# Optimization experiments

Measured on AMD Instinct MI355X. Metric: run time of the kernel, lower is better.

Reference implementation:

```python
import jax, jax.numpy as jnp
import numpy as np

N_NODES = 100000


def _graph_conv(x, W, b, src, dst, n_nodes):
    # DGL GraphConv, norm='both':
    #   h = x * out_deg(src)^{-1/2}; h = h @ W; agg = scatter_sum over dst;
    #   out = agg * in_deg(dst)^{-1/2} + b
    ones = jnp.ones(src.shape, dtype=x.dtype)
    out_deg = jax.ops.segment_sum(ones, src, num_segments=n_nodes)
    in_deg = jax.ops.segment_sum(ones, dst, num_segments=n_nodes)
    norm_src = jax.lax.rsqrt(jnp.maximum(out_deg, 1.0))  # [N]
    norm_dst = jax.lax.rsqrt(jnp.maximum(in_deg, 1.0))   # [N]
    h = (x * norm_src[:, None]) @ W                      # [N, hid]
    msgs = h[src]                                        # [E, hid] gather
    agg = jax.ops.segment_sum(msgs, dst, num_segments=n_nodes)  # [N, hid]
    return jax.nn.relu(agg * norm_dst[:, None] + b)


def setup_inputs() -> dict:
    key = jax.random.key(0)
    k1, k2, k3, k4, k5 = jax.random.split(key, 5)
    n, e, d = N_NODES, 1600000, 128
    x = jax.random.normal(k1, (n, d), dtype=jnp.float32)
    src = jax.random.randint(k2, (e,), 0, n, dtype=jnp.int32)
    dst = jax.random.randint(k3, (e,), 0, n, dtype=jnp.int32)
    # Xavier-ish init for GraphConv weights, zero bias (DGL default)
    W1 = jax.random.normal(k4, (d, d), dtype=jnp.float32) / np.sqrt(d)
    W2 = jax.random.normal(k5, (d, d), dtype=jnp.float32) / np.sqrt(d)
    b1 = jnp.zeros((d,), dtype=jnp.float32)
    b2 = jnp.zeros((d,), dtype=jnp.float32)
    return {"x": x, "W1": W1, "b1": b1, "W2": W2, "b2": b2, "src": src, "dst": dst}


def reference(x, W1, b1, W2, b2, src, dst):
    h = _graph_conv(x, W1, b1, src, dst, N_NODES)
    h = _graph_conv(h, W2, b2, src, dst, N_NODES)
    return h
```

## Files before the change

### kernel.cpp

```cpp
#include <hip/hip_runtime.h>
#include <hip/hip_fp16.h>

#define HD 128
#define CHUNK 4096
#define MAXNB 512

__global__ __launch_bounds__(256) void count_src4(const int* __restrict__ src,
                                                  unsigned int* __restrict__ cnt4s,
                                                  int N, int E) {
    int t = blockIdx.x * 256 + threadIdx.x;
    int e0 = t * 4;
    if (e0 >= E) return;
    if (e0 + 3 < E) {
        int4 s4 = ((const int4*)src)[t];
        atomicAdd(&cnt4s[0 * N + s4.x], 1u);
        atomicAdd(&cnt4s[1 * N + s4.y], 1u);
        atomicAdd(&cnt4s[2 * N + s4.z], 1u);
        atomicAdd(&cnt4s[3 * N + s4.w], 1u);
    } else {
        for (int j = 0; e0 + j < E; ++j)
            atomicAdd(&cnt4s[j * N + src[e0 + j]], 1u);
    }
}

__global__ __launch_bounds__(256) void make_norm_src(const unsigned int* __restrict__ cnt4s,
                                                     float* __restrict__ norm_src, int N) {
    int i = blockIdx.x * 256 + threadIdx.x;
    if (i < N) {
        float od = (float)(cnt4s[i] + cnt4s[N + i] + cnt4s[2 * N + i] + cnt4s[3 * N + i]);
        norm_src[i] = rsqrtf(od > 1.f ? od : 1.f);
    }
}

__global__ __launch_bounds__(256) void hist_coarse(const int* __restrict__ dst,
                                                   unsigned int* __restrict__ gHist,
                                                   int NB, int NC, int E) {
    __shared__ unsigned int hist[MAXNB];
    for (int b = threadIdx.x; b < NB; b += 256) hist[b] = 0;
    __syncthreads();
    int chunk = blockIdx.x;
    int base = chunk * CHUNK;
    int end = base + CHUNK < E ? base + CHUNK : E;
    for (int e = base + threadIdx.x; e < end; e += 256)
        atomicAdd(&hist[dst[e] >> 8], 1u);
    __syncthreads();
    for (int b = threadIdx.x; b < NB; b += 256)
        gHist[(size_t)b * NC + chunk] = hist[b];
}

__global__ __launch_bounds__(256) void scan_a(const unsigned int* __restrict__ cnt,
                                              unsigned int* __restrict__ excl,
                                              unsigned int* __restrict__ bsum, int n) {
    int i = blockIdx.x * 256 + threadIdx.x;
    unsigned int v = (i < n) ? cnt[i] : 0u;
    unsigned int x = v;
#pragma unroll
    for (int d = 1; d < 64; d <<= 1) {
        unsigned int y = __shfl_up(x, d, 64);
        if ((threadIdx.x & 63) >= d) x += y;
    }
    __shared__ unsigned int wsum[4];
    if ((threadIdx.x & 63) == 63) wsum[threadIdx.x >> 6] = x;
    __syncthreads();
    unsigned int woff = 0;
    for (int w = 0; w < (int)(threadIdx.x >> 6); ++w) woff += wsum[w];
    unsigned int incl = x + woff;
    if (i < n) excl[i] = incl - v;
    if (threadIdx.x == 255) bsum[blockIdx.x] = incl;
}

__global__ __launch_bounds__(1024) void scan_b(const unsigned int* __restrict__ bsum,
                                               unsigned int* __restrict__ boff, int nb) {
    int t = threadIdx.x;
    unsigned int v = (t < nb) ? bsum[t] : 0u;
    unsigned int x = v;
#pragma unroll
    for (int d = 1; d < 64; d <<= 1) {
        unsigned int y = __shfl_up(x, d, 64);
        if ((t & 63) >= d) x += y;
    }
    __shared__ unsigned int wsum[16];
    if ((t & 63) == 63) wsum[t >> 6] = x;
    __syncthreads();
    unsigned int woff = 0;
    for (int w = 0; w < (t >> 6); ++w) woff += wsum[w];
    unsigned int incl = x + woff;
    if (t < nb) boff[t] = incl - v;
}

__global__ __launch_bounds__(256) void scan_c(unsigned int* __restrict__ excl,
                                              const unsigned int* __restrict__ boff, int n) {
    int i = blockIdx.x * 256 + threadIdx.x;
    if (i < n) excl[i] += boff[blockIdx.x];
}

__global__ __launch_bounds__(256) void scatter_coarse(const int* __restrict__ src,
                                                      const int* __restrict__ dst,
                                                      const unsigned int* __restrict__ scanA,
                                                      unsigned int* __restrict__ packed,
                                                      int NB, int NC, int E) {
    __shared__ unsigned int curs[MAXNB];
    int chunk = blockIdx.x;
    for (int b = threadIdx.x; b < NB; b += 256)
        curs[b] = scanA[(size_t)b * NC + chunk];
    __syncthreads();
    int base = chunk * CHUNK;
    int end = base + CHUNK < E ? base + CHUNK : E;
    for (int e = base + threadIdx.x; e < end; e += 256) {
        int d = dst[e];
        int s = src[e];
        unsigned int pos = atomicAdd(&curs[d >> 8], 1u);
        packed[pos] = ((unsigned int)(d & 255) << 24) | (unsigned int)s;
    }
}

__global__ __launch_bounds__(256) void fine_sort(const unsigned int* __restrict__ packed,
                                                 const unsigned int* __restrict__ scanA,
                                                 int* __restrict__ sorted_src,
                                                 unsigned int* __restrict__ offsets,
                                                 unsigned int* __restrict__ cntg,
                                                 float* __restrict__ normd,
                                                 int NB, int NC, int N, int E) {
    __shared__ unsigned int cnt[256];
    __shared__ unsigned int curs[256];
    __shared__ unsigned int wsum[4];
    int b = blockIdx.x;
    int t = threadIdx.x;
    unsigned int S = scanA[(size_t)b * NC];
    unsigned int T = (b + 1 < NB) ? scanA[(size_t)(b + 1) * NC] : (unsigned int)E;
    cnt[t] = 0;
    __syncthreads();
    for (unsigned int j = S + t; j < T; j += 256)
        atomicAdd(&cnt[packed[j] >> 24], 1u);
    __syncthreads();
    unsigned int v = cnt[t], x = v;
    int lane = t & 63;
#pragma unroll
    for (int d = 1; d < 64; d <<= 1) {
        unsigned int y = __shfl_up(x, d, 64);
        if (lane >= d) x += y;
    }
    if (lane == 63) wsum[t >> 6] = x;
    __syncthreads();
    unsigned int woff = 0;
    for (int w = 0; w < (t >> 6); ++w) woff += wsum[w];
    unsigned int ex = x - v + woff;
    curs[t] = ex;
    int node = b * 256 + t;
    if (node < N) {
        offsets[node] = S + ex;
        cntg[node] = v;
        float f = (float)v;
        normd[node] = rsqrtf(f > 1.f ? f : 1.f);
    }
    __syncthreads();
    for (unsigned int j = S + t; j < T; j += 256) {
        unsigned int p = packed[j];
        unsigned int pos = S + atomicAdd(&curs[p >> 24], 1u);
        sorted_src[pos] = (int)(p & 0xFFFFFFu);
    }
}

__global__ __launch_bounds__(256) void gemm_norm(const float* __restrict__ x,
                                                 const float* __restrict__ norm,
                                                 const float* __restrict__ W,
                                                 __half* __restrict__ h, int n) {
    __shared__ float Ws[HD * HD];
    __shared__ float xs[32][HD];
    const float4* W4 = (const float4*)W;
    float4* Ws4 = (float4*)Ws;
#pragma unroll
    for (int i = 0; i < 16; ++i)
        Ws4[threadIdx.x + 256 * i] = W4[threadIdx.x + 256 * i];

    const int tid  = threadIdx.x;
    const int row0 = blockIdx.x * 32;

    {
        int r  = tid >> 3;
        int c0 = (tid & 7) * 4;
        int row = row0 + r;
        float nrm = (row < n) ? norm[row] : 0.f;
        const float4* xr = (const float4*)(x + (size_t)row * HD);
        float4* xd = (float4*)xs[r];
#pragma unroll
        for (int j = 0; j < 4; ++j) {
            float4 v = (row < n) ? xr[c0 + j] : make_float4(0.f, 0.f, 0.f, 0.f);
            v.x *= nrm; v.y *= nrm; v.z *= nrm; v.w *= nrm;
            xd[c0 + j] = v;
        }
    }
    __syncthreads();

    const int g  = tid >> 5;
    const int c4 = tid & 31;

    float4 a0 = make_float4(0.f,0.f,0.f,0.f), a1 = a0, a2 = a0, a3 = a0;
#pragma unroll 4
    for (int k = 0; k < HD; ++k) {
        float4 wv = Ws4[k * 32 + c4];
        float x0 = xs[g * 4 + 0][k];
        float x1 = xs[g * 4 + 1][k];
        float x2 = xs[g * 4 + 2][k];
        float x3 = xs[g * 4 + 3][k];
        a0.x = fmaf(x0, wv.x, a0.x); a0.y = fmaf(x0, wv.y, a0.y);
        a0.z = fmaf(x0, wv.z, a0.z); a0.w = fmaf(x0, wv.w, a0.w);
        a1.x = fmaf(x1, wv.x, a1.x); a1.y = fmaf(x1, wv.y, a1.y);
        a1.z = fmaf(x1, wv.z, a1.z); a1.w = fmaf(x1, wv.w, a1.w);
        a2.x = fmaf(x2, wv.x, a2.x); a2.y = fmaf(x2, wv.y, a2.y);
        a2.z = fmaf(x2, wv.z, a2.z); a2.w = fmaf(x2, wv.w, a2.w);
        a3.x = fmaf(x3, wv.x, a3.x); a3.y = fmaf(x3, wv.y, a3.y);
        a3.z = fmaf(x3, wv.z, a3.z); a3.w = fmaf(x3, wv.w, a3.w);
    }

#pragma unroll
    for (int j = 0; j < 4; ++j) {
        int row = row0 + g * 4 + j;
        if (row >= n) break;
        float4 a = (j == 0) ? a0 : (j == 1) ? a1 : (j == 2) ? a2 : a3;
        __half2 lo = __floats2half2_rn(a.x, a.y);
        __half2 hi = __floats2half2_rn(a.z, a.w);
        uint2 pk;
        pk.x = *(unsigned int*)&lo;
        pk.y = *(unsigned int*)&hi;
        ((uint2*)(h + (size_t)row * HD))[c4] = pk;
    }
}

__global__ __launch_bounds__(256) void aggregate(const __half* __restrict__ h,
                                                 const int* __restrict__ sorted_src,
                                                 const unsigned int* __restrict__ offsets,
                                                 const unsigned int* __restrict__ cnt,
                                                 const float* __restrict__ norm_dst,
                                                 const float* __restrict__ bias,
                                                 float* __restrict__ out, int n) {
    int node = blockIdx.x * 4 + (int)(threadIdx.x >> 6);
    if (node >= n) return;
    int lane = threadIdx.x & 63;
    int g   = lane >> 4;
    int sub = lane & 15;

    unsigned int start = offsets[node];
    unsigned int deg   = cnt[node];
    const int* sp = sorted_src + start;
    const uint4* h4 = (const uint4*)h;

    float acc[8];
#pragma unroll
    for (int j = 0; j < 8; ++j) acc[j] = 0.f;

#define ACCUM(u)                                                                  \
    { float2 f;                                                                   \
      f = __half22float2(*(const __half2*)&(u).x); acc[0] += f.x; acc[1] += f.y;  \
      f = __half22float2(*(const __half2*)&(u).y); acc[2] += f.x; acc[3] += f.y;  \
      f = __half22float2(*(const __half2*)&(u).z); acc[4] += f.x; acc[5] += f.y;  \
      f = __half22float2(*(const __half2*)&(u).w); acc[6] += f.x; acc[7] += f.y; }

    unsigned int i = 0;
    for (; i + 8 <= deg; i += 8) {
        int s0 = sp[i + g];
        int s1 = sp[i + 4 + g];
        uint4 u0 = h4[(size_t)s0 * 16 + sub];
        uint4 u1 = h4[(size_t)s1 * 16 + sub];
        ACCUM(u0);
        ACCUM(u1);
    }
    for (; i < deg; i += 4) {
        if (i + g < deg) {
            int s = sp[i + g];
            uint4 u = h4[(size_t)s * 16 + sub];
            ACCUM(u);
        }
    }
#undef ACCUM

#pragma unroll
    for (int j = 0; j < 8; ++j) {
        acc[j] += __shfl_xor(acc[j], 16, 64);
        acc[j] += __shfl_xor(acc[j], 32, 64);
    }

    float nd = norm_dst[node];
    float2 bb = ((const float2*)bias)[sub * 4 + g];
    float2 o;
    o.x = fmaxf(fmaf(acc[g * 2 + 0], nd, bb.x), 0.f);
    o.y = fmaxf(fmaf(acc[g * 2 + 1], nd, bb.y), 0.f);
    ((float2*)out)[(size_t)node * 64 + sub * 4 + g] = o;
}

extern "C" void kernel_launch(void* const* d_in, const int* in_sizes, int n_in,
                              void* d_out, int out_size, void* d_ws, size_t ws_size,
                              hipStream_t stream) {
    const float* x   = (const float*)d_in[0];
    const float* W1  = (const float*)d_in[1];
    const float* b1  = (const float*)d_in[2];
    const float* W2  = (const float*)d_in[3];
    const float* b2  = (const float*)d_in[4];
    const int*   src = (const int*)d_in[5];
    const int*   dst = (const int*)d_in[6];

    const int N = in_sizes[0] / HD;
    const int E = in_sizes[5];
    float* out = (float*)d_out;

    const int NB = (N + 255) / 256;
    const int NC = (E + CHUNK - 1) / CHUNK;
    const int scanLen = NB * NC;
    const int nbS = (scanLen + 255) / 256;
    const int nbN = (N + 255) / 256;

    float*        norm_src = (float*)d_ws;
    float*        normd    = norm_src + N;
    unsigned int* cntg     = (unsigned int*)(normd + N);
    unsigned int* offsets  = cntg + N;
    unsigned int* cnt4s    = offsets + N;
    unsigned int* gHist    = cnt4s + 4 * N;
    unsigned int* scanA    = gHist + scanLen;
    unsigned int* bsum     = scanA + scanLen;
    unsigned int* boff     = bsum + 1024;
    unsigned int* packed   = boff + 1024;
    int*          sorted   = (int*)(packed + E);
    __half*       h        = (__half*)(sorted + E);

    hipMemsetAsync(cnt4s, 0, (size_t)4 * N * 4, stream);
    count_src4<<<(E / 4 + 255) / 256, 256, 0, stream>>>(src, cnt4s, N, E);
    make_norm_src<<<nbN, 256, 0, stream>>>(cnt4s, norm_src, N);
    hist_coarse<<<NC, 256, 0, stream>>>(dst, gHist, NB, NC, E);
    scan_a<<<nbS, 256, 0, stream>>>(gHist, scanA, bsum, scanLen);
    scan_b<<<1, 1024, 0, stream>>>(bsum, boff, nbS);
    scan_c<<<nbS, 256, 0, stream>>>(scanA, boff, scanLen);
    scatter_coarse<<<NC, 256, 0, stream>>>(src, dst, scanA, packed, NB, NC, E);
    fine_sort<<<NB, 256, 0, stream>>>(packed, scanA, sorted, offsets, cntg, normd, NB, NC, N, E);

    gemm_norm<<<(N + 31) / 32, 256, 0, stream>>>(x, norm_src, W1, h, N);
    aggregate<<<(N + 3) / 4, 256, 0, stream>>>(h, sorted, offsets, cntg, normd, b1, out, N);

    gemm_norm<<<(N + 31) / 32, 256, 0, stream>>>(out, norm_src, W2, h, N);
    aggregate<<<(N + 3) / 4, 256, 0, stream>>>(h, sorted, offsets, cntg, normd, b2, out, N);
}
```

Measured before the change: 389.8 us.

## Use fp16 GEMM inputs, fuse source norm into aggregation, enlarge GEMM tile

```diff
diff --git a/kernel.cpp b/kernel.cpp
--- a/kernel.cpp
+++ b/kernel.cpp
@@ -161,33 +161,54 @@
     }
 }
 
-__global__ __launch_bounds__(256) void gemm_norm(const float* __restrict__ x,
-                                                 const float* __restrict__ norm,
-                                                 const float* __restrict__ W,
-                                                 __half* __restrict__ h, int n) {
-    __shared__ float Ws[HD * HD];
-    __shared__ float xs[32][HD];
-    const float4* W4 = (const float4*)W;
-    float4* Ws4 = (float4*)Ws;
-#pragma unroll
-    for (int i = 0; i < 16; ++i)
-        Ws4[threadIdx.x + 256 * i] = W4[threadIdx.x + 256 * i];
-
-    const int tid  = threadIdx.x;
-    const int row0 = blockIdx.x * 32;
+__global__ __launch_bounds__(256) void prep_x(const float* __restrict__ x,
+                                              const float* __restrict__ norm,
+                                              __half* __restrict__ xh, int total) {
+    int t = blockIdx.x * 256 + threadIdx.x;
+    if (t >= total) return;
+    int row = t >> 5;
+    float nr = norm[row];
+    float4 v = ((const float4*)x)[t];
+    __half2 lo = __floats2half2_rn(v.x * nr, v.y * nr);
+    __half2 hi = __floats2half2_rn(v.z * nr, v.w * nr);
+    uint2 pk;
+    pk.x = *(unsigned int*)&lo;
+    pk.y = *(unsigned int*)&hi;
+    ((uint2*)xh)[t] = pk;
+}
+
+__global__ __launch_bounds__(256) void gemm_h(const __half* __restrict__ xh,
+                                              const float* __restrict__ W,
+                                              __half* __restrict__ h, int n) {
+    __shared__ __half2 Wh[HD * 64];
+    __shared__ float  xs[64][HD];
+    const int tid = threadIdx.x;
 
     {
-        int r  = tid >> 3;
-        int c0 = (tid & 7) * 4;
-        int row = row0 + r;
-        float nrm = (row < n) ? norm[row] : 0.f;
-        const float4* xr = (const float4*)(x + (size_t)row * HD);
-        float4* xd = (float4*)xs[r];
-#pragma unroll
-        for (int j = 0; j < 4; ++j) {
-            float4 v = (row < n) ? xr[c0 + j] : make_float4(0.f, 0.f, 0.f, 0.f);
-            v.x *= nrm; v.y *= nrm; v.z *= nrm; v.w *= nrm;
-            xd[c0 + j] = v;
+        const float4* W4 = (const float4*)W;
+#pragma unroll
+        for (int i = 0; i < 16; ++i) {
+            int idx = tid + 256 * i;
+            float4 wv = W4[idx];
+            __half2 a = __floats2half2_rn(wv.x, wv.y);
+            __half2 b = __floats2half2_rn(wv.z, wv.w);
+            int k = idx >> 5, c4 = idx & 31;
+            Wh[k * 64 + c4 * 2]     = a;
+            Wh[k * 64 + c4 * 2 + 1] = b;
+        }
+    }
+    const int row0 = blockIdx.x * 64;
+    {
+#pragma unroll
+        for (int i = 0; i < 8; ++i) {
+            int idx = i * 256 + tid;
+            int r = idx >> 5, c = idx & 31;
+            int row = row0 + r;
+            uint2 u = make_uint2(0u, 0u);
+            if (row < n) u = ((const uint2*)xh)[(size_t)row * 32 + c];
+            float2 f0 = __half22float2(*(const __half2*)&u.x);
+            float2 f1 = __half22float2(*(const __half2*)&u.y);
+            ((float4*)xs[r])[c] = make_float4(f0.x, f0.y, f1.x, f1.y);
         }
     }
     __syncthreads();
@@ -195,45 +216,55 @@
     const int g  = tid >> 5;
     const int c4 = tid & 31;
 
-    float4 a0 = make_float4(0.f,0.f,0.f,0.f), a1 = a0, a2 = a0, a3 = a0;
-#pragma unroll 4
-    for (int k = 0; k < HD; ++k) {
-        float4 wv = Ws4[k * 32 + c4];
-        float x0 = xs[g * 4 + 0][k];
-        float x1 = xs[g * 4 + 1][k];
-        float x2 = xs[g * 4 + 2][k];
-        float x3 = xs[g * 4 + 3][k];
-        a0.x = fmaf(x0, wv.x, a0.x); a0.y = fmaf(x0, wv.y, a0.y);
-        a0.z = fmaf(x0, wv.z, a0.z); a0.w = fmaf(x0, wv.w, a0.w);
-        a1.x = fmaf(x1, wv.x, a1.x); a1.y = fmaf(x1, wv.y, a1.y);
-        a1.z = fmaf(x1, wv.z, a1.z); a1.w = fmaf(x1, wv.w, a1.w);
-        a2.x = fmaf(x2, wv.x, a2.x); a2.y = fmaf(x2, wv.y, a2.y);
-        a2.z = fmaf(x2, wv.z, a2.z); a2.w = fmaf(x2, wv.w, a2.w);
-        a3.x = fmaf(x3, wv.x, a3.x); a3.y = fmaf(x3, wv.y, a3.y);
-        a3.z = fmaf(x3, wv.z, a3.z); a3.w = fmaf(x3, wv.w, a3.w);
-    }
-
-#pragma unroll
-    for (int j = 0; j < 4; ++j) {
-        int row = row0 + g * 4 + j;
-        if (row >= n) break;
-        float4 a = (j == 0) ? a0 : (j == 1) ? a1 : (j == 2) ? a2 : a3;
-        __half2 lo = __floats2half2_rn(a.x, a.y);
-        __half2 hi = __floats2half2_rn(a.z, a.w);
-        uint2 pk;
-        pk.x = *(unsigned int*)&lo;
-        pk.y = *(unsigned int*)&hi;
-        ((uint2*)(h + (size_t)row * HD))[c4] = pk;
-    }
-}
-
-__global__ __launch_bounds__(256) void aggregate(const __half* __restrict__ h,
-                                                 const int* __restrict__ sorted_src,
-                                                 const unsigned int* __restrict__ offsets,
-                                                 const unsigned int* __restrict__ cnt,
-                                                 const float* __restrict__ norm_dst,
-                                                 const float* __restrict__ bias,
-                                                 float* __restrict__ out, int n) {
+    float4 acc[8];
+#pragma unroll
+    for (int j = 0; j < 8; ++j) acc[j] = make_float4(0.f, 0.f, 0.f, 0.f);
+
+    for (int k = 0; k < HD; k += 2) {
+        uint2 w0 = *(const uint2*)&Wh[k * 64 + c4 * 2];
+        uint2 w1 = *(const uint2*)&Wh[(k + 1) * 64 + c4 * 2];
+        float2 wa0 = __half22float2(*(const __half2*)&w0.x);
+        float2 wb0 = __half22float2(*(const __half2*)&w0.y);
+        float2 wa1 = __half22float2(*(const __half2*)&w1.x);
+        float2 wb1 = __half22float2(*(const __half2*)&w1.y);
+#pragma unroll
+        for (int j = 0; j < 8; ++j) {
+            float2 xk = *(const float2*)&xs[g * 8 + j][k];
+            acc[j].x = fmaf(xk.x, wa0.x, acc[j].x);
+            acc[j].y = fmaf(xk.x, wa0.y, acc[j].y);
+            acc[j].z = fmaf(xk.x, wb0.x, acc[j].z);
+            acc[j].w = fmaf(xk.x, wb0.y, acc[j].w);
+            acc[j].x = fmaf(xk.y, wa1.x, acc[j].x);
+            acc[j].y = fmaf(xk.y, wa1.y, acc[j].y);
+            acc[j].z = fmaf(xk.y, wb1.x, acc[j].z);
+            acc[j].w = fmaf(xk.y, wb1.y, acc[j].w);
+        }
+    }
+
+#pragma unroll
+    for (int j = 0; j < 8; ++j) {
+        int row = row0 + g * 8 + j;
+        if (row < n) {
+            __half2 lo = __floats2half2_rn(acc[j].x, acc[j].y);
+            __half2 hi = __floats2half2_rn(acc[j].z, acc[j].w);
+            uint2 pk;
+            pk.x = *(unsigned int*)&lo;
+            pk.y = *(unsigned int*)&hi;
+            ((uint2*)(h + (size_t)row * HD))[c4] = pk;
+        }
+    }
+}
+
+template <bool MID>
+__global__ __launch_bounds__(256) void aggregate_k(const __half* __restrict__ h,
+                                                   const int* __restrict__ sorted_src,
+                                                   const unsigned int* __restrict__ offsets,
+                                                   const unsigned int* __restrict__ cnt,
+                                                   const float* __restrict__ norm_dst,
+                                                   const float* __restrict__ nsrc,
+                                                   const float* __restrict__ bias,
+                                                   float* __restrict__ outF,
+                                                   __half* __restrict__ outH, int n) {
     int node = blockIdx.x * 4 + (int)(threadIdx.x >> 6);
     if (node >= n) return;
     int lane = threadIdx.x & 63;
@@ -257,13 +288,19 @@
       f = __half22float2(*(const __half2*)&(u).w); acc[6] += f.x; acc[7] += f.y; }
 
     unsigned int i = 0;
-    for (; i + 8 <= deg; i += 8) {
+    for (; i + 16 <= deg; i += 16) {
         int s0 = sp[i + g];
         int s1 = sp[i + 4 + g];
+        int s2 = sp[i + 8 + g];
+        int s3 = sp[i + 12 + g];
         uint4 u0 = h4[(size_t)s0 * 16 + sub];
         uint4 u1 = h4[(size_t)s1 * 16 + sub];
+        uint4 u2 = h4[(size_t)s2 * 16 + sub];
+        uint4 u3 = h4[(size_t)s3 * 16 + sub];
         ACCUM(u0);
         ACCUM(u1);
+        ACCUM(u2);
+        ACCUM(u3);
     }
     for (; i < deg; i += 4) {
         if (i + g < deg) {
@@ -281,11 +318,17 @@
     }
 
     float nd = norm_dst[node];
-    float2 bb = ((const float2*)bias)[sub * 4 + g];
-    float2 o;
-    o.x = fmaxf(fmaf(acc[g * 2 + 0], nd, bb.x), 0.f);
-    o.y = fmaxf(fmaf(acc[g * 2 + 1], nd, bb.y), 0.f);
-    ((float2*)out)[(size_t)node * 64 + sub * 4 + g] = o;
+    int col2 = sub * 4 + g;
+    float2 bb = ((const float2*)bias)[col2];
+    float vx = fmaxf(fmaf(acc[g * 2 + 0], nd, bb.x), 0.f);
+    float vy = fmaxf(fmaf(acc[g * 2 + 1], nd, bb.y), 0.f);
+    if (MID) {
+        float ns = nsrc[node];
+        __half2 p = __floats2half2_rn(vx * ns, vy * ns);
+        ((__half2*)outH)[(size_t)node * 64 + col2] = p;
+    } else {
+        ((float2*)outF)[(size_t)node * 64 + col2] = make_float2(vx, vy);
+    }
 }
 
 extern "C" void kernel_launch(void* const* d_in, const int* in_sizes, int n_in,
@@ -321,6 +364,7 @@
     unsigned int* packed   = boff + 1024;
     int*          sorted   = (int*)(packed + E);
     __half*       h        = (__half*)(sorted + E);
+    __half*       xh       = h + (size_t)N * HD;
 
     hipMemsetAsync(cnt4s, 0, (size_t)4 * N * 4, stream);
     count_src4<<<(E / 4 + 255) / 256, 256, 0, stream>>>(src, cnt4s, N, E);
@@ -332,9 +376,12 @@
     scatter_coarse<<<NC, 256, 0, stream>>>(src, dst, scanA, packed, NB, NC, E);
     fine_sort<<<NB, 256, 0, stream>>>(packed, scanA, sorted, offsets, cntg, normd, NB, NC, N, E);
 
-    gemm_norm<<<(N + 31) / 32, 256, 0, stream>>>(x, norm_src, W1, h, N);
-    aggregate<<<(N + 3) / 4, 256, 0, stream>>>(h, sorted, offsets, cntg, normd, b1, out, N);
-
-    gemm_norm<<<(N + 31) / 32, 256, 0, stream>>>(out, norm_src, W2, h, N);
-    aggregate<<<(N + 3) / 4, 256, 0, stream>>>(h, sorted, offsets, cntg, normd, b2, out, N);
-}
+    prep_x<<<(N * 32 + 255) / 256, 256, 0, stream>>>(x, norm_src, xh, N * 32);
+    gemm_h<<<(N + 63) / 64, 256, 0, stream>>>(xh, W1, h, N);
+    aggregate_k<true><<<(N + 3) / 4, 256, 0, stream>>>(h, sorted, offsets, cntg, normd,
+                                                       norm_src, b1, nullptr, xh, N);
+
+    gemm_h<<<(N + 63) / 64, 256, 0, stream>>>(xh, W2, h, N);
+    aggregate_k<false><<<(N + 3) / 4, 256, 0, stream>>>(h, sorted, offsets, cntg, normd,
+                                                        nullptr, b2, out, nullptr, N);
+}
```

Result: slower. 398.3 us (+2.2%).
